# Optimization experiments

Hardware: AMD Instinct MI355X
Metric: run time of the kernel (lower is better)

## Reference

```python
import jax, jax.numpy as jnp
import numpy as np
import math

SQRT32 = math.sqrt(32.0)


def _l2norm(x, eps=1e-12):
    # matches torch.nn.functional.normalize(dim=-1): x / max(||x||, eps)
    n = jnp.linalg.norm(x, axis=-1, keepdims=True)
    return x / jnp.maximum(n, eps)


def setup_inputs() -> dict:
    key = jax.random.key(0)
    k1, k2 = jax.random.split(key)
    z = jax.random.normal(k1, (8, 256, 32, 32), dtype=jnp.float32)
    # trunc_normal_(std=0.02) init approximated by scaled normal
    embed_weight = jax.random.normal(k2, (16384, 256), dtype=jnp.float32) * 0.02
    return {"z": z, "embed_weight": embed_weight}


def reference(z, embed_weight):
    # z: [b, d, h, w] channel-first -> pack to [b*h*w, d]
    b, d, h, w = z.shape
    zf = jnp.transpose(z, (0, 2, 3, 1)).reshape(-1, d)  # [N, d]

    # l2_norm=True, no predefined codebook: distance = -z @ normalize(E)^T
    ew = _l2norm(embed_weight)                          # [K, d]
    dist = -(zf @ ew.T)                                 # [N, K]
    min_encoding_indices = jnp.argmin(dist, axis=1)     # [N]

    # gather UNnormalized embedding rows, then normalize (as in source)
    z_q = _l2norm(embed_weight[min_encoding_indices])   # [N, d]

    # straight-through estimator
    z_q = zf + jax.lax.stop_gradient(z_q - zf)

    loss = jnp.zeros((1,), dtype=z.dtype)

    # unpack to [b, h, w, d]
    zq_bhwd = z_q.reshape(b, h, w, d)
    # torch .long() truncates toward zero; astype(int) does the same
    bit_indices = (zq_bhwd * SQRT32).astype(jnp.int32) + 4
    zq_out = jnp.transpose(zq_bhwd, (0, 3, 1, 2))       # [b, d, h, w]

    return zq_out, min_encoding_indices, bit_indices, loss
```

## Files before the change

### kernel.cpp

```cpp
#include <hip/hip_runtime.h>
#include <math.h>

#define D      256
#define K      16384
#define NPTS   8192
#define DELTA  0.2f
#define LCAP   2048
#define MAXCAP 4000000u

#define O_IDX  2097152
#define O_BIT  2105344
#define O_LOSS 4202496

typedef __attribute__((ext_vector_type(8))) short bf16x8;
typedef __attribute__((ext_vector_type(4))) float f32x4;
typedef unsigned long long u64;

__device__ __forceinline__ unsigned f2s(float f) {
    unsigned u = __float_as_uint(f);
    return (u & 0x80000000u) ? ~u : (u | 0x80000000u);
}
__device__ __forceinline__ float s2f(unsigned s) {
    return __uint_as_float((s & 0x80000000u) ? (s & 0x7fffffffu) : ~s);
}
__device__ __forceinline__ unsigned short f2bf(float f) {
    unsigned u = __float_as_uint(f);
    u += 0x7fffu + ((u >> 16) & 1u);
    return (unsigned short)(u >> 16);
}

__device__ __forceinline__ void gload16(const unsigned short* g, unsigned short* l) {
    __builtin_amdgcn_global_load_lds(
        (const __attribute__((address_space(1))) unsigned int*)g,
        (__attribute__((address_space(3))) unsigned int*)l, 16, 0, 0);
}

__device__ __forceinline__ unsigned lds_off(const void* p) {
    return (unsigned)(size_t)(const __attribute__((address_space(3))) void*)p;
}


__global__ __launch_bounds__(256) void prep(const float* __restrict__ E,
                                            const float* __restrict__ z,
                                            float* __restrict__ den,
                                            unsigned short* __restrict__ ewbT,
                                            unsigned short* __restrict__ zfbT,
                                            float* __restrict__ zf32,
                                            unsigned* __restrict__ gmax,
                                            u64* __restrict__ keys,
                                            unsigned* __restrict__ cnt) {
    const int blk = blockIdx.x, tid = threadIdx.x;
    if (blk < 512) {
        const int lane = tid & 63, wave = tid >> 6;
        if (blk < 32)        gmax[blk * 256 + tid] = 0u;
        else if (blk < 64)   keys[(blk - 32) * 256 + tid] = 0ull;
        else if (blk == 64 && tid < 2) cnt[tid] = 0u;
        #pragma unroll
        for (int j = 0; j < 8; ++j) {
            const int row = blk * 32 + wave * 8 + j;
            const float4 v = *(const float4*)(E + (size_t)row * D + lane * 4);
            float ss = v.x * v.x + v.y * v.y + v.z * v.z + v.w * v.w;
            #pragma unroll
            for (int o = 1; o < 64; o <<= 1) ss += __shfl_xor(ss, o);
            const float dn = fmaxf(sqrtf(ss), 1e-12f);
            const unsigned lo = (unsigned)f2bf(v.x / dn) | ((unsigned)f2bf(v.y / dn) << 16);
            const unsigned hi = (unsigned)f2bf(v.z / dn) | ((unsigned)f2bf(v.w / dn) << 16);
            *(uint2*)(ewbT + ((size_t)(lane >> 1) * K + row) * 8 + (lane & 1) * 4)
                = make_uint2(lo, hi);
            if (lane == 0) den[row] = dn;
        }
    } else {
        const int bi = blk - 512;
        const int b = bi >> 4, hw0 = (bi & 15) * 64;
        __shared__ float t[64][65];
        for (int dc = 0; dc < D; dc += 64) {
            #pragma unroll
            for (int it = 0; it < 16; ++it) {
                const int idx = it * 256 + tid;
                const int dl = idx >> 6, hw = idx & 63;
                t[dl][hw] = z[(size_t)(b * 256 + dc + dl) * 1024 + hw0 + hw];
            }
            __syncthreads();
            #pragma unroll
            for (int it = 0; it < 16; ++it) {
                const int idx = it * 256 + tid;
                const int pl = idx >> 6, dl = idx & 63;
                const float v = t[dl][pl];
                const int p = b * 1024 + hw0 + pl, k = dc + dl;
                zfbT[((size_t)(k >> 3) * NPTS + p) * 8 + (k & 7)] = f2bf(v);
                zf32[(size_t)p * D + k] = v;
            }
            __syncthreads();
        }
    }
}


#define STAGE(buf, t)                                                               \
    do {                                                                            \
        const size_t oA_ = (size_t)(t) * (8u * NPTS * 8);                           \
        const size_t oB_ = (size_t)(t) * (8u * K * 8);                              \
        unsigned short* dA_ = &sA[buf][0][0][0];                                    \
        unsigned short* dB_ = &sB[buf][0][0][0];                                    \
        gload16(gA0_ + oA_, dA_ + (size_t)tid * 8);                                 \
        gload16(gA1_ + oA_, dA_ + (size_t)(512 + tid) * 8);                         \
        gload16(gA2_ + oA_, dA_ + (size_t)(1024 + tid) * 8);                        \
        gload16(gA3_ + oA_, dA_ + (size_t)(1536 + tid) * 8);                        \
        gload16(gB0_ + oB_, dB_ + (size_t)tid * 8);                                 \
        gload16(gB1_ + oB_, dB_ + (size_t)(512 + tid) * 8);                         \
        gload16(gB2_ + oB_, dB_ + (size_t)(1024 + tid) * 8);                        \
        gload16(gB3_ + oB_, dB_ + (size_t)(1536 + tid) * 8);                        \
    } while (0)

#define RKK(buf, AA, BB)                                                            \
    do {                                                                            \
        const unsigned a__ = (AA) + (unsigned)((buf) * 32768);                      \
        const unsigned b__ = (BB) + (unsigned)((buf) * 32768);                      \
        asm volatile("ds_read_b128 %0, %1"             : "=v"(af_[0]) : "v"(a__));  \
        asm volatile("ds_read_b128 %0, %1 offset:256"  : "=v"(af_[1]) : "v"(a__));  \
        asm volatile("ds_read_b128 %0, %1 offset:512"  : "=v"(af_[2]) : "v"(a__));  \
        asm volatile("ds_read_b128 %0, %1 offset:768"  : "=v"(af_[3]) : "v"(a__));  \
        asm volatile("ds_read_b128 %0, %1 offset:1024" : "=v"(af_[4]) : "v"(a__));  \
        asm volatile("ds_read_b128 %0, %1 offset:1280" : "=v"(af_[5]) : "v"(a__));  \
        asm volatile("ds_read_b128 %0, %1 offset:1536" : "=v"(af_[6]) : "v"(a__));  \
        asm volatile("ds_read_b128 %0, %1 offset:1792" : "=v"(af_[7]) : "v"(a__));  \
        asm volatile("ds_read_b128 %0, %1"             : "=v"(bf_[0]) : "v"(b__));  \
        asm volatile("ds_read_b128 %0, %1 offset:256"  : "=v"(bf_[1]) : "v"(b__));  \
        asm volatile("ds_read_b128 %0, %1 offset:512"  : "=v"(bf_[2]) : "v"(b__));  \
        asm volatile("ds_read_b128 %0, %1 offset:768"  : "=v"(bf_[3]) : "v"(b__));  \
    } while (0)

#define LGKM_SB                                                                     \
    asm volatile("s_waitcnt lgkmcnt(0)" ::: "memory");                              \
    __builtin_amdgcn_sched_barrier(0);

#define MFMAS                                                                       \
    do {                                                                            \
        __builtin_amdgcn_s_setprio(1);                                              \
        _Pragma("unroll")                                                           \
        for (int mt = 0; mt < 8; ++mt)                                              \
            _Pragma("unroll")                                                       \
            for (int nt = 0; nt < 4; ++nt)                                          \
                acc[mt][nt] = __builtin_amdgcn_mfma_f32_16x16x32_bf16(af_[mt], bf_[nt], \
                                                                      acc[mt][nt], 0, 0, 0); \
        __builtin_amdgcn_s_setprio(0);                                              \
    } while (0)

#define WAITBAR(VM)                                                                 \
    asm volatile("s_waitcnt vmcnt(" VM ")" ::: "memory");                           \
    __builtin_amdgcn_s_barrier();                                                   \
    asm volatile("" ::: "memory");

#define BARFENCE                                                                    \
    __builtin_amdgcn_s_barrier();                                                   \
    asm volatile("" ::: "memory");

#define GEMM_CORE()                                                                 \
    __shared__ unsigned short sA[2][8][256][8];                                     \
    __shared__ unsigned short sB[2][8][256][8];                                     \
    f32x4 acc[8][4];                                                                \
    _Pragma("unroll")                                                               \
    for (int i_ = 0; i_ < 8; ++i_)                                                  \
        _Pragma("unroll")                                                           \
        for (int j_ = 0; j_ < 4; ++j_) acc[i_][j_] = (f32x4){0.f, 0.f, 0.f, 0.f};   \
    bf16x8 af_[8], bf_[4];                                                          \
    const int th_ = tid & 255, hi_ = tid >> 8;                                      \
    const int c0_ = hi_, c1_ = 2 + hi_, c2_ = 4 + hi_, c3_ = 6 + hi_;               \
    const unsigned short* gA0_ = zfbT + ((size_t)c0_ * NPTS + m0 + (th_ ^ (c0_ << 1))) * 8; \
    const unsigned short* gA1_ = zfbT + ((size_t)c1_ * NPTS + m0 + (th_ ^ (c1_ << 1))) * 8; \
    const unsigned short* gA2_ = zfbT + ((size_t)c2_ * NPTS + m0 + (th_ ^ (c2_ << 1))) * 8; \
    const unsigned short* gA3_ = zfbT + ((size_t)c3_ * NPTS + m0 + (th_ ^ (c3_ << 1))) * 8; \
    const unsigned short* gB0_ = ewbT + ((size_t)c0_ * K + n0 + (th_ ^ (c0_ << 1))) * 8; \
    const unsigned short* gB1_ = ewbT + ((size_t)c1_ * K + n0 + (th_ ^ (c1_ << 1))) * 8; \
    const unsigned short* gB2_ = ewbT + ((size_t)c2_ * K + n0 + (th_ ^ (c2_ << 1))) * 8; \
    const unsigned short* gB3_ = ewbT + ((size_t)c3_ * K + n0 + (th_ ^ (c3_ << 1))) * 8; \
    const unsigned sAb_ = lds_off(&sA[0][0][0][0]);                                 \
    const unsigned sBb_ = lds_off(&sB[0][0][0][0]);                                 \
    const int ck0_ = quad, ck1_ = 4 + quad;                                         \
    const unsigned aA0_ = sAb_ + (unsigned)((ck0_ * 256 + ((wm * 128 + col) ^ (ck0_ << 1))) * 16); \
    const unsigned aA1_ = sAb_ + (unsigned)((ck1_ * 256 + ((wm * 128 + col) ^ (ck1_ << 1))) * 16); \
    const unsigned bB0_ = sBb_ + (unsigned)((ck0_ * 256 + ((wn * 64 + col) ^ (ck0_ << 1))) * 16); \
    const unsigned bB1_ = sBb_ + (unsigned)((ck1_ * 256 + ((wn * 64 + col) ^ (ck1_ << 1))) * 16); \
    STAGE(0, 0);                                                                    \
    STAGE(1, 1);                                                                    \
    WAITBAR("8")                                                                    \
    RKK(0, aA0_, bB0_); LGKM_SB; MFMAS;                                             \
    RKK(0, aA1_, bB1_); LGKM_SB; BARFENCE; STAGE(0, 2); MFMAS;                      \
    WAITBAR("8")                                                                    \
    RKK(1, aA0_, bB0_); LGKM_SB; MFMAS;                                             \
    RKK(1, aA1_, bB1_); LGKM_SB; BARFENCE; STAGE(1, 3); MFMAS;                      \
    WAITBAR("8")                                                                    \
    RKK(0, aA0_, bB0_); LGKM_SB; MFMAS;                                             \
    RKK(0, aA1_, bB1_); LGKM_SB; MFMAS;                                             \
    WAITBAR("0")                                                                    \
    RKK(1, aA0_, bB0_); LGKM_SB; MFMAS;                                             \
    RKK(1, aA1_, bB1_); LGKM_SB; MFMAS;

#define CAND_APPEND(e)                                                              \
    do {                                                                            \
        const u64 am_ = __builtin_amdgcn_read_exec();                               \
        const unsigned n_ = (unsigned)__popcll(am_);                                \
        const unsigned rk_ = (unsigned)__popcll(am_ & ((1ull << lane) - 1));        \
        unsigned base_ = 0;                                                         \
        if (rk_ == 0) base_ = atomicAdd(cnt, n_);                                   \
        base_ = (unsigned)__builtin_amdgcn_readfirstlane((int)base_);               \
        const unsigned g_ = base_ + rk_;                                            \
        if (g_ < cap) cand[g_] = (e);                                               \
    } while (0)

#define XCD_DECODE(NT0)                                                             \
    const unsigned bid_ = blockIdx.x;                                               \
    const unsigned j_ = bid_ >> 3;                                                  \
    const int m0 = (int)(((bid_ & 7u) << 2) | (j_ & 3u)) * 256;                     \
    const int n0 = (NT0) + (int)(j_ >> 2) * 256;

__global__ __launch_bounds__(512, 2) void score_seed(const unsigned short* __restrict__ zfbT,
                                                     const unsigned short* __restrict__ ewbT,
                                                     unsigned* __restrict__ gmax,
                                                     u64* __restrict__ cand,
                                                     unsigned* __restrict__ cnt,
                                                     unsigned cap) {
    __shared__ unsigned thrS[256];
    __shared__ u64 lbuf[LCAP];
    __shared__ unsigned lcount, lbase;

    const int tid = threadIdx.x, lane = tid & 63, wave = tid >> 6;
    const int quad = lane >> 4, col = lane & 15;
    const int wm = wave >> 2, wn = wave & 3;
    XCD_DECODE(0)
    const int shsrc = lane & 48;

    if (tid < 256) thrS[tid] = 0u;
    if (tid == 0) lcount = 0u;

    GEMM_CORE()
    __syncthreads();

    float red[8][4];
    #pragma unroll
    for (int mt = 0; mt < 8; ++mt)
        #pragma unroll
        for (int r = 0; r < 4; ++r)
            red[mt][r] = fmaxf(fmaxf(acc[mt][0][r], acc[mt][1][r]),
                               fmaxf(acc[mt][2][r], acc[mt][3][r]));
    #pragma unroll
    for (int off = 1; off < 16; off <<= 1)
        #pragma unroll
        for (int mt = 0; mt < 8; ++mt)
            #pragma unroll
            for (int r = 0; r < 4; ++r)
                red[mt][r] = fmaxf(red[mt][r], __shfl_xor(red[mt][r], off));
    #pragma unroll
    for (int mt = 0; mt < 8; ++mt)
        #pragma unroll
        for (int r = 0; r < 4; ++r) {
            const int pl = wm * 128 + mt * 16 + quad * 4 + r;
            unsigned cur = 0;
            if (col == 0) {
                const unsigned enc = f2s(red[mt][r]);
                const unsigned old = atomicMax(&thrS[pl], enc);
                cur = old > enc ? old : enc;
            }
            cur = (unsigned)__shfl((int)cur, shsrc);
            red[mt][r] = s2f(cur) - DELTA;
        }

    const int ncode0 = n0 + wn * 64 + col;
    #pragma unroll
    for (int mt = 0; mt < 8; ++mt) {
        #pragma unroll
        for (int r = 0; r < 4; ++r) {
            const float tp = red[mt][r];
            const unsigned pt = m0 + wm * 128 + mt * 16 + quad * 4 + r;
            #pragma unroll
            for (int nt = 0; nt < 4; ++nt) {
                const float v = acc[mt][nt][r];
                if (v >= tp) {
                    const unsigned slot = atomicAdd(&lcount, 1u);
                    const u64 e = ((u64)((pt << 14) | (unsigned)(ncode0 + nt * 16)) << 32)
                                  | f2s(v);
                    if (slot < LCAP) lbuf[slot] = e;
                    else CAND_APPEND(e);
                }
            }
        }
    }

    __syncthreads();
    if (tid < 256) atomicMax(&gmax[m0 + tid], thrS[tid]);
    const unsigned m_ = lcount < LCAP ? lcount : LCAP;
    if (tid == 0) lbase = atomicAdd(cnt, m_);
    __syncthreads();
    for (unsigned i = tid; i < m_; i += 512) {
        const unsigned g = lbase + i;
        if (g < cap) cand[g] = lbuf[i];
    }
}

__global__ __launch_bounds__(512, 2) void score_main(const unsigned short* __restrict__ zfbT,
                                                     const unsigned short* __restrict__ ewbT,
                                                     const unsigned* __restrict__ gmax,
                                                     u64* __restrict__ cand,
                                                     unsigned* __restrict__ cnt,
                                                     unsigned cap) {
    __shared__ float thrL[256];
    __shared__ u64 lbuf[LCAP];
    __shared__ unsigned lcount, lbase;

    const int tid = threadIdx.x, lane = tid & 63, wave = tid >> 6;
    const int quad = lane >> 4, col = lane & 15;
    const int wm = wave >> 2, wn = wave & 3;
    XCD_DECODE(2048)

    if (tid < 256) thrL[tid] = s2f(gmax[m0 + tid]) - DELTA;
    if (tid == 0) lcount = 0u;

    GEMM_CORE()
    __syncthreads();

    const int ncode0 = n0 + wn * 64 + col;
    #pragma unroll
    for (int mt = 0; mt < 8; ++mt) {
        #pragma unroll
        for (int r = 0; r < 4; ++r) {
            const int pl = wm * 128 + mt * 16 + quad * 4 + r;
            const float tp = thrL[pl];
            #pragma unroll
            for (int nt = 0; nt < 4; ++nt) {
                const float v = acc[mt][nt][r];
                if (v >= tp) {
                    const unsigned slot = atomicAdd(&lcount, 1u);
                    const u64 e = ((u64)(((unsigned)pl + m0) << 14 | (unsigned)(ncode0 + nt * 16)) << 32)
                                  | f2s(v);
                    if (slot < LCAP) lbuf[slot] = e;
                    else CAND_APPEND(e);
                }
            }
        }
    }

    __syncthreads();
    const unsigned m_ = lcount < LCAP ? lcount : LCAP;
    if (tid == 0) lbase = atomicAdd(cnt, m_);
    __syncthreads();
    for (unsigned i = tid; i < m_; i += 512) {
        const unsigned g = lbase + i;
        if (g < cap) cand[g] = lbuf[i];
    }
}

__global__ __launch_bounds__(256) void cand_max(const u64* __restrict__ cand,
                                                const unsigned* __restrict__ cnt,
                                                unsigned* __restrict__ gmax,
                                                unsigned cap) {
    const unsigned total = min(cnt[0], cap);
    const unsigned stride = gridDim.x * 256;
    for (unsigned i = blockIdx.x * 256 + threadIdx.x; i < total; i += stride) {
        const u64 e = cand[i];
        atomicMax(&gmax[(unsigned)(e >> 46)], (unsigned)(e & 0xffffffffull));
    }
}

__global__ __launch_bounds__(256) void rescore(const float* __restrict__ zf32,
                                               const float* __restrict__ E,
                                               const float* __restrict__ den,
                                               const unsigned* __restrict__ gmax,
                                               const u64* __restrict__ cand,
                                               const unsigned* __restrict__ cnt,
                                               u64* __restrict__ keys,
                                               unsigned cap) {
    const unsigned total = min(cnt[0], cap);
    const int lane = threadIdx.x & 63;
    const unsigned w = (blockIdx.x * 256 + threadIdx.x) >> 6;
    const unsigned nw = gridDim.x * 4;
    for (unsigned base = w * 64; base < total; base += nw * 64) {
        const unsigned i = base + lane;
        u64 e = 0;
        bool keep = false;
        if (i < total) {
            e = cand[i];
            const int p = (int)(e >> 46);
            keep = (s2f((unsigned)(e & 0xffffffffull)) >= s2f(gmax[p]) - DELTA);
        }
        u64 mask = __ballot(keep);
        while (mask) {
            const int src = __ffsll((long long)mask) - 1;
            mask &= mask - 1;
            const unsigned pc = (unsigned)__shfl((int)(unsigned)(e >> 32), src);
            const int p = pc >> 14, c = pc & 16383;
            const float dinv = 1.0f / den[c];
            const float4 a = *(const float4*)(zf32 + (size_t)p * D + lane * 4);
            const float4 b = *(const float4*)(E + (size_t)c * D + lane * 4);
            float sv = fmaf(a.x, b.x * dinv, fmaf(a.y, b.y * dinv,
                       fmaf(a.z, b.z * dinv, a.w * (b.w * dinv))));
            #pragma unroll
            for (int o = 1; o < 64; o <<= 1) sv += __shfl_xor(sv, o);
            if (lane == 0)
                atomicMax(keys + p, ((u64)f2s(sv) << 32) | (unsigned)(16383 - c));
        }
    }
}

__global__ __launch_bounds__(256) void finalize(const float* __restrict__ E,
                                                const float* __restrict__ den,
                                                const u64* __restrict__ keys,
                                                float* __restrict__ out) {
    __shared__ float t[32][257];
    __shared__ int sIdx[32];
    __shared__ float sDen[32];
    const int tid = threadIdx.x;
    const int n0 = blockIdx.x * 32;
    if (tid < 32) {
        const u64 key = keys[n0 + tid];
        const int idx = 16383 - (int)(unsigned)(key & 0xffffffffull);
        sIdx[tid] = idx;
        sDen[tid] = den[idx];
        out[O_IDX + n0 + tid] = (float)idx;
    }
    __syncthreads();
    const float S = 5.65685424949238019520675489683895f;
    #pragma unroll 4
    for (int i = 0; i < 32; ++i) {
        const float v = E[(size_t)sIdx[i] * D + tid] / sDen[i];
        t[i][tid] = v;
        out[O_BIT + (size_t)(n0 + i) * D + tid] = (float)((int)(v * S) + 4);
    }
    __syncthreads();
    const int b = n0 >> 10, hw0 = n0 & 1023;
    const int hwl = tid & 31, cg = tid >> 5;
    #pragma unroll 4
    for (int cc = 0; cc < 32; ++cc) {
        const int c = cc * 8 + cg;
        out[(size_t)(b * 256 + c) * 1024 + hw0 + hwl] = t[hwl][c];
    }
    if (n0 == 0 && tid == 0) out[O_LOSS] = 0.0f;
}

extern "C" void kernel_launch(void* const* d_in, const int* in_sizes, int n_in,
                              void* d_out, int out_size, void* d_ws, size_t ws_size,
                              hipStream_t stream) {
    const float* z = (const float*)d_in[0];
    const float* E = (const float*)d_in[1];
    float* out = (float*)d_out;

    char* w = (char*)d_ws;
    unsigned short* ewbT = (unsigned short*)w;  w += (size_t)K * D * 2;
    unsigned short* zfbT = (unsigned short*)w;  w += (size_t)NPTS * D * 2;
    float*          zf32 = (float*)w;           w += (size_t)NPTS * D * 4;
    u64*            keys = (u64*)w;             w += (size_t)NPTS * 8;
    float*          den  = (float*)w;           w += (size_t)K * 4;
    unsigned*       gmax = (unsigned*)w;        w += (size_t)NPTS * 4;
    unsigned*       cnt  = (unsigned*)w;        w += 256;
    u64*            cand = (u64*)w;
    const size_t fixed = (size_t)(w - (char*)d_ws);
    const size_t avail = ws_size > fixed ? (ws_size - fixed) / 8 : 0;
    const unsigned cap = (unsigned)(avail < (size_t)MAXCAP ? avail : (size_t)MAXCAP);

    prep<<<640, 256, 0, stream>>>(E, z, den, ewbT, zfbT, zf32, gmax, keys, cnt);

    score_seed<<<256, 512, 0, stream>>>(zfbT, ewbT, gmax, cand, cnt, cap);
    score_main<<<1792, 512, 0, stream>>>(zfbT, ewbT, gmax, cand, cnt, cap);

    cand_max<<<256, 256, 0, stream>>>(cand, cnt, gmax, cap);
    rescore<<<1024, 256, 0, stream>>>(zf32, E, den, gmax, cand, cnt, keys, cap);
    finalize<<<NPTS / 32, 256, 0, stream>>>(E, den, keys, out);
}
```

Measured before the change: 234.5 us.

## Restructure GEMM main loop into finer-grained interleaved load/read/MFMA phases

```diff
diff --git a/kernel.cpp b/kernel.cpp
--- a/kernel.cpp
+++ b/kernel.cpp
@@ -96,64 +96,64 @@
 }
 
 
-#define STAGE(buf, t)                                                               \
-    do {                                                                            \
-        const size_t oA_ = (size_t)(t) * (8u * NPTS * 8);                           \
-        const size_t oB_ = (size_t)(t) * (8u * K * 8);                              \
-        unsigned short* dA_ = &sA[buf][0][0][0];                                    \
-        unsigned short* dB_ = &sB[buf][0][0][0];                                    \
-        gload16(gA0_ + oA_, dA_ + (size_t)tid * 8);                                 \
-        gload16(gA1_ + oA_, dA_ + (size_t)(512 + tid) * 8);                         \
-        gload16(gA2_ + oA_, dA_ + (size_t)(1024 + tid) * 8);                        \
-        gload16(gA3_ + oA_, dA_ + (size_t)(1536 + tid) * 8);                        \
-        gload16(gB0_ + oB_, dB_ + (size_t)tid * 8);                                 \
-        gload16(gB1_ + oB_, dB_ + (size_t)(512 + tid) * 8);                         \
-        gload16(gB2_ + oB_, dB_ + (size_t)(1024 + tid) * 8);                        \
-        gload16(gB3_ + oB_, dB_ + (size_t)(1536 + tid) * 8);                        \
-    } while (0)
-
-#define RKK(buf, AA, BB)                                                            \
-    do {                                                                            \
-        const unsigned a__ = (AA) + (unsigned)((buf) * 32768);                      \
-        const unsigned b__ = (BB) + (unsigned)((buf) * 32768);                      \
-        asm volatile("ds_read_b128 %0, %1"             : "=v"(af_[0]) : "v"(a__));  \
-        asm volatile("ds_read_b128 %0, %1 offset:256"  : "=v"(af_[1]) : "v"(a__));  \
-        asm volatile("ds_read_b128 %0, %1 offset:512"  : "=v"(af_[2]) : "v"(a__));  \
-        asm volatile("ds_read_b128 %0, %1 offset:768"  : "=v"(af_[3]) : "v"(a__));  \
-        asm volatile("ds_read_b128 %0, %1 offset:1024" : "=v"(af_[4]) : "v"(a__));  \
-        asm volatile("ds_read_b128 %0, %1 offset:1280" : "=v"(af_[5]) : "v"(a__));  \
-        asm volatile("ds_read_b128 %0, %1 offset:1536" : "=v"(af_[6]) : "v"(a__));  \
-        asm volatile("ds_read_b128 %0, %1 offset:1792" : "=v"(af_[7]) : "v"(a__));  \
-        asm volatile("ds_read_b128 %0, %1"             : "=v"(bf_[0]) : "v"(b__));  \
-        asm volatile("ds_read_b128 %0, %1 offset:256"  : "=v"(bf_[1]) : "v"(b__));  \
-        asm volatile("ds_read_b128 %0, %1 offset:512"  : "=v"(bf_[2]) : "v"(b__));  \
-        asm volatile("ds_read_b128 %0, %1 offset:768"  : "=v"(bf_[3]) : "v"(b__));  \
-    } while (0)
-
-#define LGKM_SB                                                                     \
-    asm volatile("s_waitcnt lgkmcnt(0)" ::: "memory");                              \
-    __builtin_amdgcn_sched_barrier(0);
-
-#define MFMAS                                                                       \
+#define SBAR  __builtin_amdgcn_sched_barrier(0);
+#define BARR  __builtin_amdgcn_s_barrier();
+#define VMC(N) asm volatile("s_waitcnt vmcnt(" N ")");
+#define LGKM_SB  asm volatile("s_waitcnt lgkmcnt(0)"); __builtin_amdgcn_sched_barrier(0);
+
+#define STG_A(slot, t, kk)                                                          \
+    do {                                                                            \
+        const int cA1_ = (kk) * 4 + hi_, cA2_ = (kk) * 4 + 2 + hi_;                 \
+        gload16(zfbT + ((size_t)((t) * 8 + cA1_) * NPTS + m0 + (th_ ^ (cA1_ << 1))) * 8, \
+                &sA[slot][cA1_][th_][0]);                                           \
+        gload16(zfbT + ((size_t)((t) * 8 + cA2_) * NPTS + m0 + (th_ ^ (cA2_ << 1))) * 8, \
+                &sA[slot][cA2_][th_][0]);                                           \
+    } while (0)
+
+#define STG_B(slot, t, kk)                                                          \
+    do {                                                                            \
+        const int cB1_ = (kk) * 4 + hi_, cB2_ = (kk) * 4 + 2 + hi_;                 \
+        gload16(ewbT + ((size_t)((t) * 8 + cB1_) * K + n0 + (th_ ^ (cB1_ << 1))) * 8, \
+                &sB[slot][cB1_][th_][0]);                                           \
+        gload16(ewbT + ((size_t)((t) * 8 + cB2_) * K + n0 + (th_ ^ (cB2_ << 1))) * 8, \
+                &sB[slot][cB2_][th_][0]);                                           \
+    } while (0)
+
+#define RD_A(slot, kO, mg)                                                          \
+    do {                                                                            \
+        const unsigned a__ = sAb_ + (unsigned)((slot) * 32768 + (mg) * 1024) + (kO);\
+        asm volatile("ds_read_b128 %0, %1"            : "=v"(af_[0]) : "v"(a__));   \
+        asm volatile("ds_read_b128 %0, %1 offset:256" : "=v"(af_[1]) : "v"(a__));   \
+        asm volatile("ds_read_b128 %0, %1 offset:512" : "=v"(af_[2]) : "v"(a__));   \
+        asm volatile("ds_read_b128 %0, %1 offset:768" : "=v"(af_[3]) : "v"(a__));   \
+    } while (0)
+
+#define RD_B(slot, kO)                                                              \
+    do {                                                                            \
+        const unsigned b__ = sBb_ + (unsigned)((slot) * 32768) + (kO);              \
+        asm volatile("ds_read_b128 %0, %1"            : "=v"(bf_[0]) : "v"(b__));   \
+        asm volatile("ds_read_b128 %0, %1 offset:256" : "=v"(bf_[1]) : "v"(b__));   \
+        asm volatile("ds_read_b128 %0, %1 offset:512" : "=v"(bf_[2]) : "v"(b__));   \
+        asm volatile("ds_read_b128 %0, %1 offset:768" : "=v"(bf_[3]) : "v"(b__));   \
+    } while (0)
+
+#define MF(mg)                                                                      \
     do {                                                                            \
         __builtin_amdgcn_s_setprio(1);                                              \
         _Pragma("unroll")                                                           \
-        for (int mt = 0; mt < 8; ++mt)                                              \
+        for (int j_ = 0; j_ < 4; ++j_)                                              \
             _Pragma("unroll")                                                       \
-            for (int nt = 0; nt < 4; ++nt)                                          \
-                acc[mt][nt] = __builtin_amdgcn_mfma_f32_16x16x32_bf16(af_[mt], bf_[nt], \
-                                                                      acc[mt][nt], 0, 0, 0); \
+            for (int nt_ = 0; nt_ < 4; ++nt_)                                       \
+                acc[(mg) * 4 + j_][nt_] = __builtin_amdgcn_mfma_f32_16x16x32_bf16(  \
+                    af_[j_], bf_[nt_], acc[(mg) * 4 + j_][nt_], 0, 0, 0);           \
         __builtin_amdgcn_s_setprio(0);                                              \
     } while (0)
 
-#define WAITBAR(VM)                                                                 \
-    asm volatile("s_waitcnt vmcnt(" VM ")" ::: "memory");                           \
-    __builtin_amdgcn_s_barrier();                                                   \
-    asm volatile("" ::: "memory");
-
-#define BARFENCE                                                                    \
-    __builtin_amdgcn_s_barrier();                                                   \
-    asm volatile("" ::: "memory");
+#define KTILE(slot, SA0, SB0, SA1, SB1, V1, V2)                                     \
+    RD_A(slot, aOff0_, 0); RD_B(slot, bOff0_); SA0; SBAR BARR LGKM_SB MF(0); SBAR BARR SBAR \
+    RD_A(slot, aOff0_, 1);                     SB0; SBAR BARR LGKM_SB MF(1); SBAR VMC(V1) BARR SBAR \
+    RD_A(slot, aOff1_, 0); RD_B(slot, bOff1_); SA1; SBAR BARR LGKM_SB MF(0); SBAR BARR SBAR \
+    RD_A(slot, aOff1_, 1);                     SB1; SBAR BARR LGKM_SB MF(1); SBAR V2 BARR SBAR
 
 #define GEMM_CORE()                                                                 \
     __shared__ unsigned short sA[2][8][256][8];                                     \
@@ -163,38 +163,22 @@
     for (int i_ = 0; i_ < 8; ++i_)                                                  \
         _Pragma("unroll")                                                           \
         for (int j_ = 0; j_ < 4; ++j_) acc[i_][j_] = (f32x4){0.f, 0.f, 0.f, 0.f};   \
-    bf16x8 af_[8], bf_[4];                                                          \
+    bf16x8 af_[4], bf_[4];                                                          \
     const int th_ = tid & 255, hi_ = tid >> 8;                                      \
-    const int c0_ = hi_, c1_ = 2 + hi_, c2_ = 4 + hi_, c3_ = 6 + hi_;               \
-    const unsigned short* gA0_ = zfbT + ((size_t)c0_ * NPTS + m0 + (th_ ^ (c0_ << 1))) * 8; \
-    const unsigned short* gA1_ = zfbT + ((size_t)c1_ * NPTS + m0 + (th_ ^ (c1_ << 1))) * 8; \
-    const unsigned short* gA2_ = zfbT + ((size_t)c2_ * NPTS + m0 + (th_ ^ (c2_ << 1))) * 8; \
-    const unsigned short* gA3_ = zfbT + ((size_t)c3_ * NPTS + m0 + (th_ ^ (c3_ << 1))) * 8; \
-    const unsigned short* gB0_ = ewbT + ((size_t)c0_ * K + n0 + (th_ ^ (c0_ << 1))) * 8; \
-    const unsigned short* gB1_ = ewbT + ((size_t)c1_ * K + n0 + (th_ ^ (c1_ << 1))) * 8; \
-    const unsigned short* gB2_ = ewbT + ((size_t)c2_ * K + n0 + (th_ ^ (c2_ << 1))) * 8; \
-    const unsigned short* gB3_ = ewbT + ((size_t)c3_ * K + n0 + (th_ ^ (c3_ << 1))) * 8; \
+    const int aRow_ = wm * 128 + col, bRow_ = wn * 64 + col;                        \
     const unsigned sAb_ = lds_off(&sA[0][0][0][0]);                                 \
     const unsigned sBb_ = lds_off(&sB[0][0][0][0]);                                 \
     const int ck0_ = quad, ck1_ = 4 + quad;                                         \
-    const unsigned aA0_ = sAb_ + (unsigned)((ck0_ * 256 + ((wm * 128 + col) ^ (ck0_ << 1))) * 16); \
-    const unsigned aA1_ = sAb_ + (unsigned)((ck1_ * 256 + ((wm * 128 + col) ^ (ck1_ << 1))) * 16); \
-    const unsigned bB0_ = sBb_ + (unsigned)((ck0_ * 256 + ((wn * 64 + col) ^ (ck0_ << 1))) * 16); \
-    const unsigned bB1_ = sBb_ + (unsigned)((ck1_ * 256 + ((wn * 64 + col) ^ (ck1_ << 1))) * 16); \
-    STAGE(0, 0);                                                                    \
-    STAGE(1, 1);                                                                    \
-    WAITBAR("8")                                                                    \
-    RKK(0, aA0_, bB0_); LGKM_SB; MFMAS;                                             \
-    RKK(0, aA1_, bB1_); LGKM_SB; BARFENCE; STAGE(0, 2); MFMAS;                      \
-    WAITBAR("8")                                                                    \
-    RKK(1, aA0_, bB0_); LGKM_SB; MFMAS;                                             \
-    RKK(1, aA1_, bB1_); LGKM_SB; BARFENCE; STAGE(1, 3); MFMAS;                      \
-    WAITBAR("8")                                                                    \
-    RKK(0, aA0_, bB0_); LGKM_SB; MFMAS;                                             \
-    RKK(0, aA1_, bB1_); LGKM_SB; MFMAS;                                             \
-    WAITBAR("0")                                                                    \
-    RKK(1, aA0_, bB0_); LGKM_SB; MFMAS;                                             \
-    RKK(1, aA1_, bB1_); LGKM_SB; MFMAS;
+    const unsigned aOff0_ = (unsigned)((ck0_ * 256 + (aRow_ ^ (ck0_ << 1))) * 16);  \
+    const unsigned aOff1_ = (unsigned)((ck1_ * 256 + (aRow_ ^ (ck1_ << 1))) * 16);  \
+    const unsigned bOff0_ = (unsigned)((ck0_ * 256 + (bRow_ ^ (ck0_ << 1))) * 16);  \
+    const unsigned bOff1_ = (unsigned)((ck1_ * 256 + (bRow_ ^ (ck1_ << 1))) * 16);  \
+    STG_A(0, 0, 0); STG_B(0, 0, 0); STG_A(0, 0, 1); STG_B(0, 0, 1);                 \
+    SBAR VMC("4") BARR SBAR                                                         \
+    KTILE(0, STG_A(1, 1, 0), STG_B(1, 1, 0), STG_A(1, 1, 1), STG_B(1, 1, 1), "4", VMC("4")) \
+    KTILE(1, STG_A(0, 2, 0), STG_B(0, 2, 0), STG_A(0, 2, 1), STG_B(0, 2, 1), "4", VMC("4")) \
+    KTILE(0, STG_A(1, 3, 0), STG_B(1, 3, 0), STG_A(1, 3, 1), STG_B(1, 3, 1), "4", VMC("4")) \
+    KTILE(1, , , , , "0", )
 
 #define CAND_APPEND(e)                                                              \
     do {                                                                            \
```

After: 232.9 us. No clear change (-0.7%).
